# Performance work log

Hardware: AMD Instinct MI355X
Metric: run time of the kernel (lower is better)

Reference implementation:

```python
import jax, jax.numpy as jnp
import numpy as np

NUM_HASHES = 3
EMBED_DIM = 256
K = 100000          # vocab-size
RATIO = 10          # hash-ratio
B_TABLE = K // RATIO  # 10000; embedding table has B_TABLE + 1 rows
BATCH, SEQ = 32, 2048


def setup_inputs() -> dict:
    key = jax.random.key(0)
    k1, k2, k3 = jax.random.split(key, 3)
    x = jax.random.randint(k1, (BATCH, SEQ, NUM_HASHES), 0, K, dtype=jnp.int64) \
        if jax.config.jax_enable_x64 else \
        jax.random.randint(k1, (BATCH, SEQ, NUM_HASHES), 0, K).astype(jnp.int32)
    emb_table = jax.random.normal(k2, (B_TABLE + 1, EMBED_DIM), dtype=jnp.float32)
    weight_table = jax.random.normal(k3, (K * NUM_HASHES + NUM_HASHES, 1), dtype=jnp.float32)
    return {"x": x, "emb_table": emb_table, "weight_table": weight_table}


def reference(x, emb_table, weight_table):
    # x: [B, S, H] token hashes in [0, K)
    indices = x // RATIO                                   # [B, S, H] -> rows of emb_table
    hash_offsets = (jnp.arange(NUM_HASHES) * (K + 1)).astype(x.dtype)
    weight_idx = x + hash_offsets                          # per-hash salted weight index
    w = weight_table[weight_idx, 0]                        # [B, S, H] per-sample weights
    e = emb_table[indices]                                 # [B, S, H, D] gathered embeddings
    # EmbeddingBag(mode='sum', per_sample_weights): weighted sum over the hash dim
    out = jnp.einsum('bshd,bsh->bsd', e, w)                # [B, S, D]
    return out
```

## Files before the change

kernel.cpp:

```cpp
#include <hip/hip_runtime.h>


#define NUM_HASHES 3
#define EMBED_DIM 256
#define KVOCAB 100000
#define RATIO 10
#define NROWS (KVOCAB / RATIO + 1)
#define QTAB_BYTES ((size_t)NROWS * EMBED_DIM)
#define WS_NEED (QTAB_BYTES + (size_t)NROWS * 4)

typedef float f32x4 __attribute__((ext_vector_type(4)));

__device__ __forceinline__ float sbyte_f(unsigned int p, int j) {
    return (float)((signed char)(p >> (8 * j)));
}

__global__ __launch_bounds__(256) void quant_rows_i8(
    const float* __restrict__ emb,
    signed char* __restrict__ qt,
    float*       __restrict__ scales,
    int nrows)
{
    const int row = blockIdx.x * 4 + (threadIdx.x >> 6);
    if (row >= nrows) return;
    const int lane = threadIdx.x & 63;

    f32x4 v = __builtin_nontemporal_load(
        reinterpret_cast<const f32x4*>(emb + (size_t)row * EMBED_DIM) + lane);
    float m = fmaxf(fmaxf(fabsf(v.x), fabsf(v.y)), fmaxf(fabsf(v.z), fabsf(v.w)));
#pragma unroll
    for (int off = 32; off; off >>= 1)
        m = fmaxf(m, __shfl_xor(m, off, 64));

    const float s  = m * (1.0f / 127.0f);
    const float rs = (m > 0.f) ? (127.0f / m) : 0.f;

    const int qx = (int)rintf(v.x * rs);
    const int qy = (int)rintf(v.y * rs);
    const int qz = (int)rintf(v.z * rs);
    const int qw = (int)rintf(v.w * rs);
    const unsigned int packed = (qx & 0xff) | ((qy & 0xff) << 8) |
                                ((qz & 0xff) << 16) | ((qw & 0xff) << 24);
    reinterpret_cast<unsigned int*>(qt + (size_t)row * EMBED_DIM)[lane] = packed;
    if (lane == 0) scales[row] = s;
}

__global__ __launch_bounds__(256) void hash_emb_i8x4(
    const int*         __restrict__ x,
    const signed char* __restrict__ qt,
    const float*       __restrict__ scales,
    const float*       __restrict__ wt,
    float*             __restrict__ out,
    int T)
{
    int tb = ((blockIdx.x * 256 + threadIdx.x) >> 6) * 4;
    if (tb >= T) return;
    tb = __builtin_amdgcn_readfirstlane(tb);
    const int lane = threadIdx.x & 63;

    const int* xp = x + (size_t)tb * NUM_HASHES;
    int xv[12];
#pragma unroll
    for (int i = 0; i < 12; ++i) xv[i] = xp[i];

    unsigned int p[4][3];
    int idx[4][3];
#pragma unroll
    for (int t = 0; t < 4; ++t)
#pragma unroll
        for (int h = 0; h < NUM_HASHES; ++h) {
            idx[t][h] = (int)((unsigned)xv[t * 3 + h] / RATIO);
            p[t][h] = reinterpret_cast<const unsigned int*>(
                          qt + (size_t)idx[t][h] * EMBED_DIM)[lane];
        }

    float ws[4][3];
#pragma unroll
    for (int t = 0; t < 4; ++t)
#pragma unroll
        for (int h = 0; h < NUM_HASHES; ++h)
            ws[t][h] = wt[xv[t * 3 + h] + h * (KVOCAB + 1)] * scales[idx[t][h]];

#pragma unroll
    for (int t = 0; t < 4; ++t) {
        f32x4 acc;
        acc.x = sbyte_f(p[t][0], 0) * ws[t][0] + sbyte_f(p[t][1], 0) * ws[t][1] + sbyte_f(p[t][2], 0) * ws[t][2];
        acc.y = sbyte_f(p[t][0], 1) * ws[t][0] + sbyte_f(p[t][1], 1) * ws[t][1] + sbyte_f(p[t][2], 1) * ws[t][2];
        acc.z = sbyte_f(p[t][0], 2) * ws[t][0] + sbyte_f(p[t][1], 2) * ws[t][1] + sbyte_f(p[t][2], 2) * ws[t][2];
        acc.w = sbyte_f(p[t][0], 3) * ws[t][0] + sbyte_f(p[t][1], 3) * ws[t][1] + sbyte_f(p[t][2], 3) * ws[t][2];
        __builtin_nontemporal_store(acc,
            reinterpret_cast<f32x4*>(out + (size_t)(tb + t) * EMBED_DIM) + lane);
    }
}

__global__ __launch_bounds__(256) void hash_emb_f32(
    const int*   __restrict__ x,
    const float* __restrict__ emb,
    const float* __restrict__ wt,
    float*       __restrict__ out,
    int T)
{
    const int token = blockIdx.x * 4 + (threadIdx.x >> 6);
    if (token >= T) return;
    const int lane = threadIdx.x & 63;

    const int* xp = x + (size_t)token * NUM_HASHES;
    f32x4 acc = {0.f, 0.f, 0.f, 0.f};
#pragma unroll
    for (int h = 0; h < NUM_HASHES; ++h) {
        const int   xv = xp[h];
        const float wv = wt[xv + h * (KVOCAB + 1)];
        const f32x4 e  = reinterpret_cast<const f32x4*>(
                             emb + (size_t)((unsigned)xv / RATIO) * EMBED_DIM)[lane];
        acc.x += e.x * wv; acc.y += e.y * wv; acc.z += e.z * wv; acc.w += e.w * wv;
    }
    __builtin_nontemporal_store(acc,
        reinterpret_cast<f32x4*>(out + (size_t)token * EMBED_DIM) + lane);
}

extern "C" void kernel_launch(void* const* d_in, const int* in_sizes, int n_in,
                              void* d_out, int out_size, void* d_ws, size_t ws_size,
                              hipStream_t stream) {
    const int*   x   = (const int*)d_in[0];
    const float* emb = (const float*)d_in[1];
    const float* wt  = (const float*)d_in[2];
    float*       out = (float*)d_out;

    const int T = in_sizes[0] / NUM_HASHES;

    if (ws_size >= WS_NEED) {
        signed char* qt     = (signed char*)d_ws;
        float*       scales = (float*)((char*)d_ws + QTAB_BYTES);
        hipLaunchKernelGGL(quant_rows_i8, dim3((NROWS + 3) / 4), dim3(256), 0, stream,
                           emb, qt, scales, NROWS);
        const int waves  = (T + 3) / 4;
        const int blocks = (waves + 3) / 4;
        hipLaunchKernelGGL(hash_emb_i8x4, dim3(blocks), dim3(256), 0, stream,
                           x, qt, scales, wt, out, T);
    } else {
        const int blocks = (T + 3) / 4;
        hipLaunchKernelGGL(hash_emb_f32, dim3(blocks), dim3(256), 0, stream,
                           x, emb, wt, out, T);
    }
}
```

Measured before the change: 25.31 us.

## Prefetch per-sample hash weights in the quantization prologue kernel

```diff
diff --git a/kernel.cpp b/kernel.cpp
--- a/kernel.cpp
+++ b/kernel.cpp
@@ -7,7 +7,10 @@
 #define RATIO 10
 #define NROWS (KVOCAB / RATIO + 1)
 #define QTAB_BYTES ((size_t)NROWS * EMBED_DIM)
-#define WS_NEED (QTAB_BYTES + (size_t)NROWS * 4)
+#define SCALES_OFF QTAB_BYTES
+#define SCALES_BYTES ((size_t)NROWS * 4)
+#define WPREP_OFF ((SCALES_OFF + SCALES_BYTES + 255) & ~(size_t)255)
+#define QUANT_BLOCKS ((NROWS + 3) / 4)
 
 typedef float f32x4 __attribute__((ext_vector_type(4)));
 
@@ -15,41 +18,55 @@
     return (float)((signed char)(p >> (8 * j)));
 }
 
-__global__ __launch_bounds__(256) void quant_rows_i8(
+__global__ __launch_bounds__(256) void prologue(
     const float* __restrict__ emb,
+    const int*   __restrict__ x,
+    const float* __restrict__ wt,
     signed char* __restrict__ qt,
     float*       __restrict__ scales,
-    int nrows)
+    float*       __restrict__ wprep,
+    int nrows, int T)
 {
-    const int row = blockIdx.x * 4 + (threadIdx.x >> 6);
-    if (row >= nrows) return;
-    const int lane = threadIdx.x & 63;
+    if ((int)blockIdx.x < QUANT_BLOCKS) {
+        const int row = blockIdx.x * 4 + (threadIdx.x >> 6);
+        if (row >= nrows) return;
+        const int lane = threadIdx.x & 63;
 
-    f32x4 v = __builtin_nontemporal_load(
-        reinterpret_cast<const f32x4*>(emb + (size_t)row * EMBED_DIM) + lane);
-    float m = fmaxf(fmaxf(fabsf(v.x), fabsf(v.y)), fmaxf(fabsf(v.z), fabsf(v.w)));
+        f32x4 v = __builtin_nontemporal_load(
+            reinterpret_cast<const f32x4*>(emb + (size_t)row * EMBED_DIM) + lane);
+        float m = fmaxf(fmaxf(fabsf(v.x), fabsf(v.y)), fmaxf(fabsf(v.z), fabsf(v.w)));
 #pragma unroll
-    for (int off = 32; off; off >>= 1)
-        m = fmaxf(m, __shfl_xor(m, off, 64));
+        for (int off = 32; off; off >>= 1)
+            m = fmaxf(m, __shfl_xor(m, off, 64));
 
-    const float s  = m * (1.0f / 127.0f);
-    const float rs = (m > 0.f) ? (127.0f / m) : 0.f;
+        const float s  = m * (1.0f / 127.0f);
+        const float rs = (m > 0.f) ? (127.0f / m) : 0.f;
 
-    const int qx = (int)rintf(v.x * rs);
-    const int qy = (int)rintf(v.y * rs);
-    const int qz = (int)rintf(v.z * rs);
-    const int qw = (int)rintf(v.w * rs);
-    const unsigned int packed = (qx & 0xff) | ((qy & 0xff) << 8) |
-                                ((qz & 0xff) << 16) | ((qw & 0xff) << 24);
-    reinterpret_cast<unsigned int*>(qt + (size_t)row * EMBED_DIM)[lane] = packed;
-    if (lane == 0) scales[row] = s;
+        const int qx = (int)rintf(v.x * rs);
+        const int qy = (int)rintf(v.y * rs);
+        const int qz = (int)rintf(v.z * rs);
+        const int qw = (int)rintf(v.w * rs);
+        const unsigned int packed = (qx & 0xff) | ((qy & 0xff) << 8) |
+                                    ((qz & 0xff) << 16) | ((qw & 0xff) << 24);
+        reinterpret_cast<unsigned int*>(qt + (size_t)row * EMBED_DIM)[lane] = packed;
+        if (lane == 0) scales[row] = s;
+    } else {
+        const int t = ((int)blockIdx.x - QUANT_BLOCKS) * 256 + (int)threadIdx.x;
+        if (t >= T) return;
+        const int xv0 = x[(size_t)t * 3 + 0];
+        const int xv1 = x[(size_t)t * 3 + 1];
+        const int xv2 = x[(size_t)t * 3 + 2];
+        wprep[(size_t)t * 3 + 0] = wt[xv0];
+        wprep[(size_t)t * 3 + 1] = wt[xv1 + (KVOCAB + 1)];
+        wprep[(size_t)t * 3 + 2] = wt[xv2 + 2 * (KVOCAB + 1)];
+    }
 }
 
-__global__ __launch_bounds__(256) void hash_emb_i8x4(
+__global__ __launch_bounds__(256) void hash_emb_main(
     const int*         __restrict__ x,
     const signed char* __restrict__ qt,
     const float*       __restrict__ scales,
-    const float*       __restrict__ wt,
+    const float*       __restrict__ wprep,
     float*             __restrict__ out,
     int T)
 {
@@ -58,10 +75,13 @@
     tb = __builtin_amdgcn_readfirstlane(tb);
     const int lane = threadIdx.x & 63;
 
-    const int* xp = x + (size_t)tb * NUM_HASHES;
-    int xv[12];
+    const int*   xp = x     + (size_t)tb * 3;
+    const float* wp = wprep + (size_t)tb * 3;
+
+    int   xv[12];
+    float w[12];
 #pragma unroll
-    for (int i = 0; i < 12; ++i) xv[i] = xp[i];
+    for (int i = 0; i < 12; ++i) { xv[i] = xp[i]; w[i] = wp[i]; }
 
     unsigned int p[4][3];
     int idx[4][3];
@@ -79,7 +99,7 @@
     for (int t = 0; t < 4; ++t)
 #pragma unroll
         for (int h = 0; h < NUM_HASHES; ++h)
-            ws[t][h] = wt[xv[t * 3 + h] + h * (KVOCAB + 1)] * scales[idx[t][h]];
+            ws[t][h] = w[t * 3 + h] * scales[idx[t][h]];
 
 #pragma unroll
     for (int t = 0; t < 4; ++t) {
@@ -127,16 +147,22 @@
     float*       out = (float*)d_out;
 
     const int T = in_sizes[0] / NUM_HASHES;
+    const size_t wprep_bytes = (size_t)T * 3 * 4;
+    const size_t ws_need = WPREP_OFF + wprep_bytes;
 
-    if (ws_size >= WS_NEED) {
+    if (ws_size >= ws_need) {
         signed char* qt     = (signed char*)d_ws;
-        float*       scales = (float*)((char*)d_ws + QTAB_BYTES);
-        hipLaunchKernelGGL(quant_rows_i8, dim3((NROWS + 3) / 4), dim3(256), 0, stream,
-                           emb, qt, scales, NROWS);
+        float*       scales = (float*)((char*)d_ws + SCALES_OFF);
+        float*       wprep  = (float*)((char*)d_ws + WPREP_OFF);
+
+        const int prep_blocks = (T + 255) / 256;
+        hipLaunchKernelGGL(prologue, dim3(QUANT_BLOCKS + prep_blocks), dim3(256), 0, stream,
+                           emb, x, wt, qt, scales, wprep, NROWS, T);
+
         const int waves  = (T + 3) / 4;
         const int blocks = (waves + 3) / 4;
-        hipLaunchKernelGGL(hash_emb_i8x4, dim3(blocks), dim3(256), 0, stream,
-                           x, qt, scales, wt, out, T);
+        hipLaunchKernelGGL(hash_emb_main, dim3(blocks), dim3(256), 0, stream,
+                           x, qt, scales, wprep, out, T);
     } else {
         const int blocks = (T + 3) / 4;
         hipLaunchKernelGGL(hash_emb_f32, dim3(blocks), dim3(256), 0, stream,
```

Result: slower. 26.46 us (+4.6%).
